# Kernel tuning notes

Hardware: AMD Instinct MI355X
Metric: run time of the kernel (lower is better)

## Reference

```python
import jax, jax.numpy as jnp
import numpy as np

B, N, S, D = 32, 128, 64, 512
MAX_LEN = 5000


def make_pe(d_model, max_len):
    pos = np.arange(max_len, dtype=np.float32)[:, None]
    div = np.exp(np.arange(0, d_model, 2, dtype=np.float32) * (-np.log(10000.0) / d_model))
    pe = np.zeros((max_len, d_model), dtype=np.float32)
    pe[:, 0::2] = np.sin(pos * div)
    pe[:, 1::2] = np.cos(pos * div)
    return jnp.asarray(pe)


def setup_inputs() -> dict:
    key = jax.random.key(0)
    ks = jax.random.split(key, 16)
    s1 = 1.0 / np.sqrt(D)
    s2 = 1.0 / np.sqrt(2 * D)
    inp = {
        "x": jax.random.normal(ks[0], (B, N), jnp.float32),
        "timesteps": jax.random.randint(ks[1], (B,), 0, 1000),
        "fusion_feat": jax.random.normal(ks[2], (B, D), jnp.float32),
        "tar_image_feat": jax.random.normal(ks[3], (B, N, S, D), jnp.float32),
        "pe": make_pe(D, MAX_LEN),
        # torch Linear weights are [out, in]
        "Wq": jax.random.normal(ks[4], (D, D), jnp.float32) * s1,
        "Wk": jax.random.normal(ks[5], (D, D), jnp.float32) * s1,
        "Wv": jax.random.normal(ks[6], (D, D), jnp.float32) * s1,
        "Wp": jax.random.normal(ks[7], (D, D), jnp.float32) * s1,
        "bp": jnp.zeros((D,), jnp.float32),
        "Wt1": jax.random.normal(ks[8], (D, D), jnp.float32) * s1,
        "bt1": jnp.zeros((D,), jnp.float32),
        "Wt2": jax.random.normal(ks[9], (D, D), jnp.float32) * s1,
        "bt2": jnp.zeros((D,), jnp.float32),
        "Wd1": jax.random.normal(ks[10], (2 * D, 2 * D), jnp.float32) * s2,
        "bd1": jnp.zeros((2 * D,), jnp.float32),
        "Wd2": jax.random.normal(ks[11], (1, 2 * D), jnp.float32) * s2,
        "bd2": jnp.zeros((1,), jnp.float32),
    }
    return inp


def reference(x, timesteps, fusion_feat, tar_image_feat, pe,
              Wq, Wk, Wv, Wp, bp, Wt1, bt1, Wt2, bt2, Wd1, bd1, Wd2, bd2):
    # timestep embedding: pe[timesteps] -> [B, D], then 2-layer SiLU MLP (eval mode: dropout off)
    cond = jax.nn.silu(pe[timesteps] @ Wt1.T + bt1) @ Wt2.T + bt2  # [B, D]

    # similarity argmax over S tokens, then gather best token per (b, n)
    sim = jnp.einsum('bd,bnsd->bns', fusion_feat, tar_image_feat)  # [B, N, S]
    best = jnp.argmax(sim, axis=-1)                                # [B, N]
    tif = jnp.take_along_axis(tar_image_feat, best[:, :, None, None], axis=2)[:, :, 0, :]  # [B, N, D]

    # single-vector attention over N candidates
    q = (fusion_feat + cond) @ Wq.T                  # [B, D]
    k = (tif + cond[:, None, :]) @ Wk.T              # [B, N, D]
    v = (tif + cond[:, None, :]) @ Wv.T              # [B, N, D]
    w = jax.nn.softmax(jnp.einsum('bd,bnd->bn', q, k) + x, axis=-1)  # [B, N]
    new_emb = jnp.einsum('bn,bnd->bd', w, v) @ Wp.T + bp             # [B, D]

    # MLP decode over concat [new_emb (broadcast), tif]
    emb = jnp.concatenate([jnp.broadcast_to(new_emb[:, None, :], tif.shape), tif], axis=-1)  # [B, N, 2D]
    h = jax.nn.relu(emb @ Wd1.T + bd1)
    p = (h @ Wd2.T + bd2)[..., 0] + w                # [B, N]

    # sort descending along N
    return -jnp.sort(-p, axis=1)
```

## Files before the change

### kernel.cpp

```cpp
#include <hip/hip_runtime.h>
#include <hip/hip_bf16.h>
#include <math.h>


#define BB 32
#define NN 128
#define SS 64
#define DD 512

typedef __attribute__((ext_vector_type(8))) short short8;
typedef __attribute__((ext_vector_type(4))) float f32x4;

__device__ __forceinline__ ushort f2bf(float f) {
    unsigned u = __float_as_uint(f);
    unsigned r = (u + 0x7fffu + ((u >> 16) & 1u)) >> 16;
    return (ushort)r;
}

__device__ __forceinline__ void wave_dot512x4(
    const float* __restrict__ w, size_t ldw, float4 xa, float4 xb,
    int lane, float out[4]) {
    float4 ra[4], rb[4];
#pragma unroll
    for (int r = 0; r < 4; ++r) {
        const float4* row = reinterpret_cast<const float4*>(w + (size_t)r * ldw);
        ra[r] = row[lane * 2];
        rb[r] = row[lane * 2 + 1];
    }
#pragma unroll
    for (int r = 0; r < 4; ++r) {
        float s = ra[r].x * xa.x + ra[r].y * xa.y + ra[r].z * xa.z + ra[r].w * xa.w
                + rb[r].x * xb.x + rb[r].y * xb.y + rb[r].z * xb.z + rb[r].w * xb.w;
#pragma unroll
        for (int off = 32; off; off >>= 1) s += __shfl_xor(s, off);
        out[r] = s;
    }
}

__global__ __launch_bounds__(256) void bmv(
    const float* __restrict__ W, int ldw, const float* __restrict__ bias,
    const float* __restrict__ Xa, const float* __restrict__ Xb,
    const int* __restrict__ ts, const float* __restrict__ pe,
    float* __restrict__ Y, int R, int act, int mode) {
    __shared__ __align__(16) float xl[DD];
    int b = blockIdx.y, tid = threadIdx.x, lane = tid & 63, wave = tid >> 6;
    const float* src = (mode == 1) ? (pe + (size_t)ts[b] * DD) : (Xa + (size_t)b * DD);
    if (mode == 2) {
        const float* s2 = Xb + (size_t)b * DD;
        for (int i = tid; i < DD; i += 256) xl[i] = src[i] + s2[i];
    } else {
        for (int i = tid; i < DD; i += 256) xl[i] = src[i];
    }
    __syncthreads();
    float4 xa = reinterpret_cast<const float4*>(xl)[lane * 2];
    float4 xb = reinterpret_cast<const float4*>(xl)[lane * 2 + 1];
    int j0 = blockIdx.x * 16 + wave * 4;
    float s[4];
    wave_dot512x4(W + (size_t)j0 * ldw, ldw, xa, xb, lane, s);
    if (lane < 4) {
        int j = j0 + lane;
        float v = s[lane];
        if (bias) v += bias[j];
        if (act == 1) v = v / (1.f + expf(-v));
        Y[(size_t)b * R + j] = v;
    }
}

__global__ __launch_bounds__(256) void k_qk(
    const float* __restrict__ Wk, const float* __restrict__ q,
    float* __restrict__ qk) {
    __shared__ __align__(16) float ql[DD];
    __shared__ float part[4][64];
    int b = blockIdx.y, c0 = blockIdx.x * 64;
    int tid = threadIdx.x, lane = tid & 63, wave = tid >> 6;
    for (int i = tid; i < DD; i += 256) ql[i] = q[(size_t)b * DD + i];
    __syncthreads();
    float p = 0.f;
    for (int j = wave * 128; j < wave * 128 + 128; ++j)
        p += ql[j] * Wk[(size_t)j * DD + c0 + lane];
    part[wave][lane] = p;
    __syncthreads();
    if (tid < 64)
        qk[(size_t)b * DD + c0 + tid] =
            part[0][tid] + part[1][tid] + part[2][tid] + part[3][tid];
}

__global__ __launch_bounds__(256) void k2_sim(
    const float* __restrict__ fusion, const float* __restrict__ tif,
    const float* __restrict__ x, const float* __restrict__ qk,
    const float* __restrict__ Wd1, ushort* __restrict__ Wb,
    float* __restrict__ tif_best, ushort* __restrict__ abf,
    float* __restrict__ score) {
    __shared__ __align__(16) float fb[DD];
    __shared__ float bv_s[4];
    __shared__ int bi_s[4];
    __shared__ int bidx_s;
    __shared__ float dred[4];
    int bn = blockIdx.x, b = bn >> 7;
    int tid = threadIdx.x, lane = tid & 63, wave = tid >> 6;

    if (bn < 1024) {
        int idx = (bn * 256 + tid) * 2;
        int r = idx >> 9, k = idx & 511;
        float2 v = *reinterpret_cast<const float2*>(Wd1 + (size_t)r * 1024 + 512 + k);
        ushort2 o = {f2bf(v.x), f2bf(v.y)};
        *reinterpret_cast<ushort2*>(Wb + (size_t)r * 512 + k) = o;
    }

    for (int i = tid; i < DD; i += 256) fb[i] = fusion[(size_t)b * DD + i];
    __syncthreads();
    float4 xa = reinterpret_cast<const float4*>(fb)[lane * 2];
    float4 xb = reinterpret_cast<const float4*>(fb)[lane * 2 + 1];
    const float* base = tif + (size_t)bn * SS * DD;
    float bv = -INFINITY;
    int bi = 0;
    for (int s0 = wave * 16; s0 < wave * 16 + 16; s0 += 4) {
        float sv[4];
        wave_dot512x4(base + (size_t)s0 * DD, DD, xa, xb, lane, sv);
#pragma unroll
        for (int r = 0; r < 4; ++r)
            if (sv[r] > bv) { bv = sv[r]; bi = s0 + r; }
    }
    if (lane == 0) { bv_s[wave] = bv; bi_s[wave] = bi; }
    __syncthreads();
    if (tid == 0) {
        float v = bv_s[0]; int i0 = bi_s[0];
        for (int w = 1; w < 4; w++)
            if (bv_s[w] > v) { v = bv_s[w]; i0 = bi_s[w]; }
        bidx_s = i0;
    }
    __syncthreads();
    const float* src = base + (size_t)bidx_s * DD;
    const float* qkb = qk + (size_t)b * DD;
    float local = 0.f;
    for (int i = tid; i < DD; i += 256) {
        float vv = src[i];
        tif_best[(size_t)bn * DD + i] = vv;
        abf[(size_t)bn * DD + i] = f2bf(vv);
        local += vv * qkb[i];
    }
#pragma unroll
    for (int off = 32; off; off >>= 1) local += __shfl_xor(local, off);
    if (lane == 0) dred[wave] = local;
    __syncthreads();
    if (tid == 0) score[bn] = dred[0] + dred[1] + dred[2] + dred[3] + x[bn];
}

__global__ __launch_bounds__(256) void k_vsum(
    const float* __restrict__ score, const float* __restrict__ tif_best,
    const float* __restrict__ cond,
    float* __restrict__ wout, float* __restrict__ vsum) {
    __shared__ float wl[NN];
    __shared__ float redm[2], reds[2];
    int b = blockIdx.y, tid = threadIdx.x, lane = tid & 63, wave = tid >> 6;
    float v = 0.f;
    if (tid < NN) {
        v = score[b * NN + tid];
        float m = v;
#pragma unroll
        for (int off = 32; off; off >>= 1) m = fmaxf(m, __shfl_xor(m, off));
        if (lane == 0) redm[wave] = m;
    }
    __syncthreads();
    float m = fmaxf(redm[0], redm[1]);
    if (tid < NN) {
        float e = expf(v - m);
        wl[tid] = e;
        float s = e;
#pragma unroll
        for (int off = 32; off; off >>= 1) s += __shfl_xor(s, off);
        if (lane == 0) reds[wave] = s;
    }
    __syncthreads();
    float inv = 1.f / (reds[0] + reds[1]);
    if (blockIdx.x == 0 && tid < NN) wout[b * NN + tid] = wl[tid] * inv;
    int d = blockIdx.x * 256 + tid;
    const float* base = tif_best + (size_t)b * NN * DD + d;
    float s = 0.f;
#pragma unroll 8
    for (int n = 0; n < NN; n++) s += wl[n] * base[(size_t)n * DD];
    vsum[(size_t)b * DD + d] = s * inv + cond[(size_t)b * DD + d];
}

__global__ __launch_bounds__(256) void k4_mfma(
    const ushort* __restrict__ Abf, const ushort* __restrict__ Wb,
    const float* __restrict__ Wd1, const float* __restrict__ bd1,
    const float* __restrict__ ne, const float* __restrict__ Wd2,
    float* __restrict__ p_part) {
    __shared__ ushort aS[128 * 64];
    __shared__ ushort bS[128 * 64];
    __shared__ __align__(16) float nel[DD];
    __shared__ float uloc[128];
    int tid = threadIdx.x, l = tid & 63, w = tid >> 6;
    int m0 = blockIdx.x * 128, n0 = blockIdx.y * 128;
    int b = blockIdx.x;
    int wm = w >> 1, wn = w & 1;

    for (int i = tid; i < DD; i += 256) nel[i] = ne[(size_t)b * DD + i];
    __syncthreads();
    float4 na = reinterpret_cast<const float4*>(nel)[l * 2];
    float4 nb = reinterpret_cast<const float4*>(nel)[l * 2 + 1];

#define STAGE(K0)                                                              \
    {                                                                          \
        _Pragma("unroll") for (int i = 0; i < 4; ++i) {                        \
            int L = i * 4096 + w * 1024 + l * 16;                              \
            int row = L >> 7;                                                  \
            int bo = L & 127;                                                  \
            int sb = bo ^ ((row & 7) << 4);                                    \
            const ushort* ga = Abf + (size_t)(m0 + row) * DD + (K0) + (sb >> 1); \
            const ushort* gb = Wb + (size_t)(n0 + row) * DD + (K0) + (sb >> 1);  \
            __builtin_amdgcn_global_load_lds(                                  \
                (const __attribute__((address_space(1))) void*)ga,             \
                (__attribute__((address_space(3))) void*)(aS + i * 2048 + w * 512), \
                16, 0, 0);                                                     \
            __builtin_amdgcn_global_load_lds(                                  \
                (const __attribute__((address_space(1))) void*)gb,             \
                (__attribute__((address_space(3))) void*)(bS + i * 2048 + w * 512), \
                16, 0, 0);                                                     \
        }                                                                      \
    }

    STAGE(0);
    for (int j0 = 0; j0 < 32; j0 += 4) {
        int r = w * 32 + j0;
        float s[4];
        wave_dot512x4(Wd1 + (size_t)(n0 + r) * 1024, 1024, na, nb, l, s);
        if (l < 4) uloc[r + l] = s[l] + bd1[n0 + r + l];
    }
    __syncthreads();

    f32x4 acc[4][4];
#pragma unroll
    for (int i = 0; i < 4; i++)
#pragma unroll
        for (int j = 0; j < 4; j++) acc[i][j] = (f32x4){0.f, 0.f, 0.f, 0.f};

    for (int k0 = 0; k0 < DD; k0 += 64) {
#pragma unroll
        for (int kk = 0; kk < 2; ++kk) {
            short8 af[4], bf[4];
#pragma unroll
            for (int f = 0; f < 4; ++f) {
                int ra = wm * 64 + f * 16 + (l & 15);
                int boa = (((l >> 4) * 16 + kk * 64)) ^ ((ra & 7) << 4);
                af[f] = *reinterpret_cast<const short8*>(&aS[ra * 64 + (boa >> 1)]);
                int rb = wn * 64 + f * 16 + (l & 15);
                int bob = (((l >> 4) * 16 + kk * 64)) ^ ((rb & 7) << 4);
                bf[f] = *reinterpret_cast<const short8*>(&bS[rb * 64 + (bob >> 1)]);
            }
#pragma unroll
            for (int fm = 0; fm < 4; ++fm)
#pragma unroll
                for (int fn = 0; fn < 4; ++fn)
                    acc[fm][fn] = __builtin_amdgcn_mfma_f32_16x16x32_bf16(
                        af[fm], bf[fn], acc[fm][fn], 0, 0, 0);
        }
        __syncthreads();
        if (k0 + 64 < DD) {
            STAGE(k0 + 64);
            __syncthreads();
        }
    }
#undef STAGE
#pragma unroll
    for (int fm = 0; fm < 4; ++fm) {
#pragma unroll
        for (int reg = 0; reg < 4; ++reg) {
            float pp = 0.f;
#pragma unroll
            for (int fn = 0; fn < 4; ++fn) {
                int rl = wn * 64 + fn * 16 + (l & 15);
                float hh = acc[fm][fn][reg] + uloc[rl];
                if (hh > 0.f) pp += Wd2[n0 + rl] * hh;
            }
#pragma unroll
            for (int off = 1; off < 16; off <<= 1) pp += __shfl_xor(pp, off);
            if ((l & 15) == 0) {
                int m = m0 + wm * 64 + fm * 16 + (l >> 4) * 4 + reg;
                p_part[(size_t)m * 16 + blockIdx.y * 2 + wn] = pp;
            }
        }
    }
}

__global__ __launch_bounds__(128) void k5_sort(
    const float* __restrict__ p_part, const float* __restrict__ wout,
    const float* __restrict__ bd2, float* __restrict__ out) {
    __shared__ float v[NN];
    int b = blockIdx.x, tid = threadIdx.x;
    int bn = b * NN + tid;
    float s = bd2[0] + wout[bn];
#pragma unroll
    for (int c = 0; c < 16; c++) s += p_part[(size_t)bn * 16 + c];
    v[tid] = s;
    __syncthreads();
    for (int k = 2; k <= NN; k <<= 1) {
        for (int j = k >> 1; j > 0; j >>= 1) {
            int ixj = tid ^ j;
            if (ixj > tid) {
                float a = v[tid], bb2 = v[ixj];
                bool desc = (tid & k) == 0;
                if (desc ? (a < bb2) : (a > bb2)) { v[tid] = bb2; v[ixj] = a; }
            }
            __syncthreads();
        }
    }
    out[bn] = v[tid];
}

extern "C" void kernel_launch(void* const* d_in, const int* in_sizes, int n_in,
                              void* d_out, int out_size, void* d_ws, size_t ws_size,
                              hipStream_t stream) {
    const float* x      = (const float*)d_in[0];
    const int*   ts     = (const int*)d_in[1];
    const float* fusion = (const float*)d_in[2];
    const float* tif    = (const float*)d_in[3];
    const float* pe     = (const float*)d_in[4];
    const float* Wq     = (const float*)d_in[5];
    const float* Wk     = (const float*)d_in[6];
    const float* Wv     = (const float*)d_in[7];
    const float* Wp     = (const float*)d_in[8];
    const float* bp     = (const float*)d_in[9];
    const float* Wt1    = (const float*)d_in[10];
    const float* bt1    = (const float*)d_in[11];
    const float* Wt2    = (const float*)d_in[12];
    const float* bt2    = (const float*)d_in[13];
    const float* Wd1    = (const float*)d_in[14];
    const float* bd1    = (const float*)d_in[15];
    const float* Wd2    = (const float*)d_in[16];
    const float* bd2    = (const float*)d_in[17];

    float* ws = (float*)d_ws;
    float* cond     = ws;
    float* qk       = cond + 16384;
    float* h        = qk + 16384;
    float* q        = h + 16384;
    float* score    = q + 16384;
    float* wout     = score + 4096;
    float* vsum     = wout + 4096;
    float* ve       = vsum + 16384;
    float* ne       = ve + 16384;
    float* p_part   = ne + 16384;
    float* tif_best = p_part + 65536;
    ushort* Abf     = (ushort*)(tif_best + 2097152);
    ushort* Wb      = Abf + 2097152;
    float* out = (float*)d_out;

    hipLaunchKernelGGL(bmv, dim3(32, BB), dim3(256), 0, stream,
                       Wt1, DD, bt1, nullptr, nullptr, ts, pe, h, DD, 1, 1);
    hipLaunchKernelGGL(bmv, dim3(32, BB), dim3(256), 0, stream,
                       Wt2, DD, bt2, h, nullptr, nullptr, nullptr, cond, DD, 0, 0);
    hipLaunchKernelGGL(bmv, dim3(32, BB), dim3(256), 0, stream,
                       Wq, DD, nullptr, fusion, cond, nullptr, nullptr, q, DD, 0, 2);
    hipLaunchKernelGGL(k_qk, dim3(8, BB), dim3(256), 0, stream, Wk, q, qk);

    hipLaunchKernelGGL(k2_sim, dim3(BB * NN), dim3(256), 0, stream,
                       fusion, tif, x, qk, Wd1, Wb, tif_best, Abf, score);

    hipLaunchKernelGGL(k_vsum, dim3(2, BB), dim3(256), 0, stream,
                       score, tif_best, cond, wout, vsum);
    hipLaunchKernelGGL(bmv, dim3(32, BB), dim3(256), 0, stream,
                       Wv, DD, nullptr, vsum, nullptr, nullptr, nullptr, ve, DD, 0, 0);
    hipLaunchKernelGGL(bmv, dim3(32, BB), dim3(256), 0, stream,
                       Wp, DD, bp, ve, nullptr, nullptr, nullptr, ne, DD, 0, 0);

    hipLaunchKernelGGL(k4_mfma, dim3(32, 8), dim3(256), 0, stream,
                       Abf, Wb, Wd1, bd1, ne, Wd2, p_part);
    hipLaunchKernelGGL(k5_sort, dim3(BB), dim3(128), 0, stream,
                       p_part, wout, bd2, out);
}
```

Baseline: 187.4 us.

## Fuse timestep MLP and query chain into similarity kernel; double-buffer MFMA staging

The timestep MLP, query projection and q·Wk product now run inside the similarity/gather kernel, in 32 extra blocks ahead of the per-(b,n) blocks. This removes four small launches and their serial dependencies. The attention score dot products move into the softmax kernel, which reads the gathered tokens directly. The MFMA decode kernel gains a second LDS buffer so the next K tile's global→LDS loads overlap compute, trading double the LDS footprint for removing one barrier per iteration. Each of the 32 condition blocks does the full serial chain of matvecs for one batch, which could become a long tail while the other blocks run.

```diff
diff --git a/kernel.cpp b/kernel.cpp
--- a/kernel.cpp
+++ b/kernel.cpp
@@ -39,18 +39,11 @@
 
 __global__ __launch_bounds__(256) void bmv(
     const float* __restrict__ W, int ldw, const float* __restrict__ bias,
-    const float* __restrict__ Xa, const float* __restrict__ Xb,
-    const int* __restrict__ ts, const float* __restrict__ pe,
-    float* __restrict__ Y, int R, int act, int mode) {
+    const float* __restrict__ Xa, float* __restrict__ Y, int R, int act) {
     __shared__ __align__(16) float xl[DD];
     int b = blockIdx.y, tid = threadIdx.x, lane = tid & 63, wave = tid >> 6;
-    const float* src = (mode == 1) ? (pe + (size_t)ts[b] * DD) : (Xa + (size_t)b * DD);
-    if (mode == 2) {
-        const float* s2 = Xb + (size_t)b * DD;
-        for (int i = tid; i < DD; i += 256) xl[i] = src[i] + s2[i];
-    } else {
-        for (int i = tid; i < DD; i += 256) xl[i] = src[i];
-    }
+    const float* src = Xa + (size_t)b * DD;
+    for (int i = tid; i < DD; i += 256) xl[i] = src[i];
     __syncthreads();
     float4 xa = reinterpret_cast<const float4*>(xl)[lane * 2];
     float4 xb = reinterpret_cast<const float4*>(xl)[lane * 2 + 1];
@@ -66,39 +59,102 @@
     }
 }
 
-__global__ __launch_bounds__(256) void k_qk(
-    const float* __restrict__ Wk, const float* __restrict__ q,
-    float* __restrict__ qk) {
+__global__ __launch_bounds__(256) void k2_fused(
+    const int* __restrict__ ts, const float* __restrict__ pe,
+    const float* __restrict__ fusion, const float* __restrict__ tif,
+    const float* __restrict__ Wt1, const float* __restrict__ bt1,
+    const float* __restrict__ Wt2, const float* __restrict__ bt2,
+    const float* __restrict__ Wq, const float* __restrict__ Wk,
+    const float* __restrict__ Wd1, ushort* __restrict__ Wb,
+    float* __restrict__ cond, float* __restrict__ qk,
+    float* __restrict__ tif_best, ushort* __restrict__ abf) {
+    __shared__ __align__(16) float xin[DD];
+    __shared__ __align__(16) float hl[DD];
+    __shared__ __align__(16) float cl[DD];
     __shared__ __align__(16) float ql[DD];
-    __shared__ float part[4][64];
-    int b = blockIdx.y, c0 = blockIdx.x * 64;
-    int tid = threadIdx.x, lane = tid & 63, wave = tid >> 6;
-    for (int i = tid; i < DD; i += 256) ql[i] = q[(size_t)b * DD + i];
-    __syncthreads();
-    float p = 0.f;
-    for (int j = wave * 128; j < wave * 128 + 128; ++j)
-        p += ql[j] * Wk[(size_t)j * DD + c0 + lane];
-    part[wave][lane] = p;
-    __syncthreads();
-    if (tid < 64)
-        qk[(size_t)b * DD + c0 + tid] =
-            part[0][tid] + part[1][tid] + part[2][tid] + part[3][tid];
-}
-
-__global__ __launch_bounds__(256) void k2_sim(
-    const float* __restrict__ fusion, const float* __restrict__ tif,
-    const float* __restrict__ x, const float* __restrict__ qk,
-    const float* __restrict__ Wd1, ushort* __restrict__ Wb,
-    float* __restrict__ tif_best, ushort* __restrict__ abf,
-    float* __restrict__ score) {
-    __shared__ __align__(16) float fb[DD];
+    __shared__ __align__(16) float paux[4][DD >> 2];
     __shared__ float bv_s[4];
     __shared__ int bi_s[4];
     __shared__ int bidx_s;
-    __shared__ float dred[4];
-    int bn = blockIdx.x, b = bn >> 7;
-    int tid = threadIdx.x, lane = tid & 63, wave = tid >> 6;
-
+    int blk = blockIdx.x, tid = threadIdx.x, lane = tid & 63, wave = tid >> 6;
+
+    if (blk < 32) {
+        int b = blk;
+        {
+            const float* per = pe + (size_t)ts[b] * DD;
+            for (int i = tid; i < DD; i += 256) xin[i] = per[i];
+        }
+        __syncthreads();
+        {
+            float4 xa = reinterpret_cast<const float4*>(xin)[lane * 2];
+            float4 xb = reinterpret_cast<const float4*>(xin)[lane * 2 + 1];
+            for (int j0 = wave * 128; j0 < wave * 128 + 128; j0 += 4) {
+                float s[4];
+                wave_dot512x4(Wt1 + (size_t)j0 * DD, DD, xa, xb, lane, s);
+                if (lane < 4) {
+                    float v = s[lane] + bt1[j0 + lane];
+                    hl[j0 + lane] = v / (1.f + expf(-v));
+                }
+            }
+        }
+        __syncthreads();
+        {
+            float4 xa = reinterpret_cast<const float4*>(hl)[lane * 2];
+            float4 xb = reinterpret_cast<const float4*>(hl)[lane * 2 + 1];
+            for (int j0 = wave * 128; j0 < wave * 128 + 128; j0 += 4) {
+                float s[4];
+                wave_dot512x4(Wt2 + (size_t)j0 * DD, DD, xa, xb, lane, s);
+                if (lane < 4) {
+                    float v = s[lane] + bt2[j0 + lane];
+                    cl[j0 + lane] = v;
+                    cond[(size_t)b * DD + j0 + lane] = v;
+                }
+            }
+        }
+        __syncthreads();
+        for (int i = tid; i < DD; i += 256) xin[i] = fusion[(size_t)b * DD + i] + cl[i];
+        __syncthreads();
+        {
+            float4 xa = reinterpret_cast<const float4*>(xin)[lane * 2];
+            float4 xb = reinterpret_cast<const float4*>(xin)[lane * 2 + 1];
+            for (int j0 = wave * 128; j0 < wave * 128 + 128; j0 += 4) {
+                float s[4];
+                wave_dot512x4(Wq + (size_t)j0 * DD, DD, xa, xb, lane, s);
+                if (lane < 4) ql[j0 + lane] = s[lane];
+            }
+        }
+        __syncthreads();
+        {
+            float a8[8] = {0, 0, 0, 0, 0, 0, 0, 0};
+            for (int j = wave * 128; j < wave * 128 + 128; ++j) {
+                float qj = ql[j];
+                const float4* row = reinterpret_cast<const float4*>(Wk + ((size_t)j << 9));
+                float4 r0 = row[lane * 2];
+                float4 r1 = row[lane * 2 + 1];
+                a8[0] += qj * r0.x; a8[1] += qj * r0.y;
+                a8[2] += qj * r0.z; a8[3] += qj * r0.w;
+                a8[4] += qj * r1.x; a8[5] += qj * r1.y;
+                a8[6] += qj * r1.z; a8[7] += qj * r1.w;
+            }
+            if ((wave & 1) == 0) {
+#pragma unroll
+                for (int e = 0; e < 8; ++e)
+                    (wave == 0 ? hl : cl)[lane * 8 + e] = a8[e];
+            }
+            __syncthreads();
+            if (wave & 1) {
+#pragma unroll
+                for (int e = 0; e < 8; ++e)
+                    (wave == 1 ? hl : cl)[lane * 8 + e] += a8[e];
+            }
+            __syncthreads();
+            for (int c = tid; c < DD; c += 256)
+                qk[(size_t)b * DD + c] = hl[c] + cl[c];
+        }
+        return;
+    }
+
+    int bn = blk - 32, b = bn >> 7;
     if (bn < 1024) {
         int idx = (bn * 256 + tid) * 2;
         int r = idx >> 9, k = idx & 511;
@@ -106,11 +162,10 @@
         ushort2 o = {f2bf(v.x), f2bf(v.y)};
         *reinterpret_cast<ushort2*>(Wb + (size_t)r * 512 + k) = o;
     }
-
-    for (int i = tid; i < DD; i += 256) fb[i] = fusion[(size_t)b * DD + i];
-    __syncthreads();
-    float4 xa = reinterpret_cast<const float4*>(fb)[lane * 2];
-    float4 xb = reinterpret_cast<const float4*>(fb)[lane * 2 + 1];
+    for (int i = tid; i < DD; i += 256) xin[i] = fusion[(size_t)b * DD + i];
+    __syncthreads();
+    float4 xa = reinterpret_cast<const float4*>(xin)[lane * 2];
+    float4 xb = reinterpret_cast<const float4*>(xin)[lane * 2 + 1];
     const float* base = tif + (size_t)bn * SS * DD;
     float bv = -INFINITY;
     int bi = 0;
@@ -131,31 +186,36 @@
     }
     __syncthreads();
     const float* src = base + (size_t)bidx_s * DD;
-    const float* qkb = qk + (size_t)b * DD;
-    float local = 0.f;
     for (int i = tid; i < DD; i += 256) {
         float vv = src[i];
         tif_best[(size_t)bn * DD + i] = vv;
         abf[(size_t)bn * DD + i] = f2bf(vv);
-        local += vv * qkb[i];
-    }
-#pragma unroll
-    for (int off = 32; off; off >>= 1) local += __shfl_xor(local, off);
-    if (lane == 0) dred[wave] = local;
-    __syncthreads();
-    if (tid == 0) score[bn] = dred[0] + dred[1] + dred[2] + dred[3] + x[bn];
+    }
 }
 
 __global__ __launch_bounds__(256) void k_vsum(
-    const float* __restrict__ score, const float* __restrict__ tif_best,
-    const float* __restrict__ cond,
+    const float* __restrict__ qk, const float* __restrict__ x,
+    const float* __restrict__ tif_best, const float* __restrict__ cond,
     float* __restrict__ wout, float* __restrict__ vsum) {
+    __shared__ __align__(16) float qkl[DD];
     __shared__ float wl[NN];
     __shared__ float redm[2], reds[2];
     int b = blockIdx.y, tid = threadIdx.x, lane = tid & 63, wave = tid >> 6;
+    for (int i = tid; i < DD; i += 256) qkl[i] = qk[(size_t)b * DD + i];
+    __syncthreads();
+    {
+        float4 xa = reinterpret_cast<const float4*>(qkl)[lane * 2];
+        float4 xb = reinterpret_cast<const float4*>(qkl)[lane * 2 + 1];
+        for (int n0 = wave * 32; n0 < wave * 32 + 32; n0 += 4) {
+            float s[4];
+            wave_dot512x4(tif_best + ((size_t)(b * NN + n0)) * DD, DD, xa, xb, lane, s);
+            if (lane < 4) wl[n0 + lane] = s[lane] + x[b * NN + n0 + lane];
+        }
+    }
+    __syncthreads();
     float v = 0.f;
     if (tid < NN) {
-        v = score[b * NN + tid];
+        v = wl[tid];
         float m = v;
 #pragma unroll
         for (int off = 32; off; off >>= 1) m = fmaxf(m, __shfl_xor(m, off));
@@ -163,14 +223,16 @@
     }
     __syncthreads();
     float m = fmaxf(redm[0], redm[1]);
+    float e = 0.f;
     if (tid < NN) {
-        float e = expf(v - m);
-        wl[tid] = e;
+        e = expf(v - m);
         float s = e;
 #pragma unroll
         for (int off = 32; off; off >>= 1) s += __shfl_xor(s, off);
         if (lane == 0) reds[wave] = s;
     }
+    __syncthreads();
+    if (tid < NN) wl[tid] = e;
     __syncthreads();
     float inv = 1.f / (reds[0] + reds[1]);
     if (blockIdx.x == 0 && tid < NN) wout[b * NN + tid] = wl[tid] * inv;
@@ -187,8 +249,8 @@
     const float* __restrict__ Wd1, const float* __restrict__ bd1,
     const float* __restrict__ ne, const float* __restrict__ Wd2,
     float* __restrict__ p_part) {
-    __shared__ ushort aS[128 * 64];
-    __shared__ ushort bS[128 * 64];
+    __shared__ ushort aS[2][128 * 64];
+    __shared__ ushort bS[2][128 * 64];
     __shared__ __align__(16) float nel[DD];
     __shared__ float uloc[128];
     int tid = threadIdx.x, l = tid & 63, w = tid >> 6;
@@ -201,7 +263,7 @@
     float4 na = reinterpret_cast<const float4*>(nel)[l * 2];
     float4 nb = reinterpret_cast<const float4*>(nel)[l * 2 + 1];
 
-#define STAGE(K0)                                                              \
+#define STAGE(K0, BUF)                                                         \
     {                                                                          \
         _Pragma("unroll") for (int i = 0; i < 4; ++i) {                        \
             int L = i * 4096 + w * 1024 + l * 16;                              \
@@ -212,16 +274,16 @@
             const ushort* gb = Wb + (size_t)(n0 + row) * DD + (K0) + (sb >> 1);  \
             __builtin_amdgcn_global_load_lds(                                  \
                 (const __attribute__((address_space(1))) void*)ga,             \
-                (__attribute__((address_space(3))) void*)(aS + i * 2048 + w * 512), \
+                (__attribute__((address_space(3))) void*)(aS[BUF] + i * 2048 + w * 512), \
                 16, 0, 0);                                                     \
             __builtin_amdgcn_global_load_lds(                                  \
                 (const __attribute__((address_space(1))) void*)gb,             \
-                (__attribute__((address_space(3))) void*)(bS + i * 2048 + w * 512), \
+                (__attribute__((address_space(3))) void*)(bS[BUF] + i * 2048 + w * 512), \
                 16, 0, 0);                                                     \
         }                                                                      \
     }
 
-    STAGE(0);
+    STAGE(0, 0);
     for (int j0 = 0; j0 < 32; j0 += 4) {
         int r = w * 32 + j0;
         float s[4];
@@ -236,7 +298,9 @@
 #pragma unroll
         for (int j = 0; j < 4; j++) acc[i][j] = (f32x4){0.f, 0.f, 0.f, 0.f};
 
+    int cur = 0;
     for (int k0 = 0; k0 < DD; k0 += 64) {
+        if (k0 + 64 < DD) STAGE(k0 + 64, cur ^ 1);
 #pragma unroll
         for (int kk = 0; kk < 2; ++kk) {
             short8 af[4], bf[4];
@@ -244,10 +308,10 @@
             for (int f = 0; f < 4; ++f) {
                 int ra = wm * 64 + f * 16 + (l & 15);
                 int boa = (((l >> 4) * 16 + kk * 64)) ^ ((ra & 7) << 4);
-                af[f] = *reinterpret_cast<const short8*>(&aS[ra * 64 + (boa >> 1)]);
+                af[f] = *reinterpret_cast<const short8*>(&aS[cur][ra * 64 + (boa >> 1)]);
                 int rb = wn * 64 + f * 16 + (l & 15);
                 int bob = (((l >> 4) * 16 + kk * 64)) ^ ((rb & 7) << 4);
-                bf[f] = *reinterpret_cast<const short8*>(&bS[rb * 64 + (bob >> 1)]);
+                bf[f] = *reinterpret_cast<const short8*>(&bS[cur][rb * 64 + (bob >> 1)]);
             }
 #pragma unroll
             for (int fm = 0; fm < 4; ++fm)
@@ -257,10 +321,7 @@
                         af[fm], bf[fn], acc[fm][fn], 0, 0, 0);
         }
         __syncthreads();
-        if (k0 + 64 < DD) {
-            STAGE(k0 + 64);
-            __syncthreads();
-        }
+        cur ^= 1;
     }
 #undef STAGE
 #pragma unroll
@@ -334,10 +395,7 @@
     float* ws = (float*)d_ws;
     float* cond     = ws;
     float* qk       = cond + 16384;
-    float* h        = qk + 16384;
-    float* q        = h + 16384;
-    float* score    = q + 16384;
-    float* wout     = score + 4096;
+    float* wout     = qk + 16384;
     float* vsum     = wout + 4096;
     float* ve       = vsum + 16384;
     float* ne       = ve + 16384;
@@ -347,23 +405,17 @@
     ushort* Wb      = Abf + 2097152;
     float* out = (float*)d_out;
 
+    hipLaunchKernelGGL(k2_fused, dim3(32 + BB * NN), dim3(256), 0, stream,
+                       ts, pe, fusion, tif, Wt1, bt1, Wt2, bt2, Wq, Wk,
+                       Wd1, Wb, cond, qk, tif_best, Abf);
+
+    hipLaunchKernelGGL(k_vsum, dim3(2, BB), dim3(256), 0, stream,
+                       qk, x, tif_best, cond, wout, vsum);
+
     hipLaunchKernelGGL(bmv, dim3(32, BB), dim3(256), 0, stream,
-                       Wt1, DD, bt1, nullptr, nullptr, ts, pe, h, DD, 1, 1);
+                       Wv, DD, nullptr, vsum, ve, DD, 0);
     hipLaunchKernelGGL(bmv, dim3(32, BB), dim3(256), 0, stream,
-                       Wt2, DD, bt2, h, nullptr, nullptr, nullptr, cond, DD, 0, 0);
-    hipLaunchKernelGGL(bmv, dim3(32, BB), dim3(256), 0, stream,
-                       Wq, DD, nullptr, fusion, cond, nullptr, nullptr, q, DD, 0, 2);
-    hipLaunchKernelGGL(k_qk, dim3(8, BB), dim3(256), 0, stream, Wk, q, qk);
-
-    hipLaunchKernelGGL(k2_sim, dim3(BB * NN), dim3(256), 0, stream,
-                       fusion, tif, x, qk, Wd1, Wb, tif_best, Abf, score);
-
-    hipLaunchKernelGGL(k_vsum, dim3(2, BB), dim3(256), 0, stream,
-                       score, tif_best, cond, wout, vsum);
-    hipLaunchKernelGGL(bmv, dim3(32, BB), dim3(256), 0, stream,
-                       Wv, DD, nullptr, vsum, nullptr, nullptr, nullptr, ve, DD, 0, 0);
-    hipLaunchKernelGGL(bmv, dim3(32, BB), dim3(256), 0, stream,
-                       Wp, DD, bp, ve, nullptr, nullptr, nullptr, ne, DD, 0, 0);
+                       Wp, DD, bp, ve, ne, DD, 0);
 
     hipLaunchKernelGGL(k4_mfma, dim3(32, 8), dim3(256), 0, stream,
                        Abf, Wb, Wd1, bd1, ne, Wd2, p_part);
```

Result: slower. 237.0 us (+26.4%).
